# Kernel optimization log

Measured on AMD Instinct MI355X. Metric: run time of the kernel, lower is better.

## Reference

```python
import jax, jax.numpy as jnp
import numpy as np

N, L, IN = 256, 128, 8
H1, H2, OUT = 768, 512, 1


def setup_inputs() -> dict:
    key = jax.random.key(0)
    ks = jax.random.split(key, 13)
    s = 0.02
    p = lambda k, shape: jax.random.normal(k, shape, dtype=jnp.float32) * s
    return {
        "x": jax.random.normal(ks[0], (N, L, IN), dtype=jnp.float32),
        "W_ih1": p(ks[1], (4 * H1, IN + 1)),
        "b_ih1": p(ks[2], (4 * H1,)),
        "W_hh1": p(ks[3], (4 * H1, H1)),
        "b_hh1": p(ks[4], (4 * H1,)),
        "W_ih2": p(ks[5], (4 * H1, H1)),
        "b_ih2": p(ks[6], (4 * H1,)),
        "W_hh2": p(ks[7], (4 * H1, H1)),
        "b_hh2": p(ks[8], (4 * H1,)),
        "W1": p(ks[9], (H2, H1)),
        "b1": p(ks[10], (H2,)),
        "W2": p(ks[11], (OUT, H2)),
        "b2": p(ks[12], (OUT,)),
    }


def _lstm_cell(inp, h, c, W_ih, b_ih, W_hh, b_hh):
    # PyTorch LSTMCell: gates ordered (input, forget, cell, output)
    g = inp @ W_ih.T + b_ih + h @ W_hh.T + b_hh
    i, f, gg, o = jnp.split(g, 4, axis=-1)
    c = jax.nn.sigmoid(f) * c + jax.nn.sigmoid(i) * jnp.tanh(gg)
    h = jax.nn.sigmoid(o) * jnp.tanh(c)
    return h, c


def reference(x, W_ih1, b_ih1, W_hh1, b_hh1, W_ih2, b_ih2, W_hh2, b_hh2, W1, b1, W2, b2):
    Nb = x.shape[0]
    H = W_hh1.shape[1]
    z = jnp.zeros((Nb, H), x.dtype)
    col0 = jnp.zeros((Nb, 1), x.dtype)  # initial_output = initial_implied_storage = 0

    def step(carry, x_t):  # x_t: (N, IN)
        h1, c1, h2, c2, prev_out, prev_store = carry
        cur_store = prev_store + x_t[:, :1] - prev_out  # (N, 1)
        inp = jnp.concatenate([x_t, cur_store], axis=-1)  # (N, IN+1)
        h1, c1 = _lstm_cell(inp, h1, c1, W_ih1, b_ih1, W_hh1, b_hh1)
        h2, c2 = _lstm_cell(h1, h2, c2, W_ih2, b_ih2, W_hh2, b_hh2)
        # dropout_prob = 0 -> dropout layers are identity
        out = jax.nn.relu(h2 @ W1.T + b1) @ W2.T + b2  # (N, 1)
        return (h1, c1, h2, c2, out, cur_store), (out, cur_store)

    _, (outs, stores) = jax.lax.scan(step, (z, z, z, z, col0, col0), jnp.swapaxes(x, 0, 1))
    # (L, N, 1) -> (N, L, 1)
    return jnp.swapaxes(outs, 0, 1), jnp.swapaxes(stores, 0, 1)
```

## Files before the change

### kernel.cpp

```cpp
#include <hip/hip_runtime.h>

typedef unsigned short u16;
typedef unsigned int u32;
typedef __attribute__((ext_vector_type(8))) unsigned short ushort8;
typedef __attribute__((ext_vector_type(4))) float f32x4;
typedef __attribute__((ext_vector_type(2))) float f32x2;
typedef __attribute__((ext_vector_type(4))) unsigned int u32x4;
typedef __attribute__((ext_vector_type(8))) __bf16 bf16x8;

#define N_B 256
#define LSEQ 128
#define AROW 2304
#define NBLK 256

#define MFMA_B16(a, b, c) __builtin_amdgcn_mfma_f32_16x16x32_bf16( \
    __builtin_bit_cast(bf16x8, a), __builtin_bit_cast(bf16x8, b), c, 0, 0, 0)

#define GLLDS(gp, lp) __builtin_amdgcn_global_load_lds( \
    (const __attribute__((address_space(1))) void*)(gp), \
    (__attribute__((address_space(3))) void*)(lp), 16, 0, 0)
#define GLLDS_C(gp, lp) __builtin_amdgcn_global_load_lds( \
    (const __attribute__((address_space(1))) void*)(gp), \
    (__attribute__((address_space(3))) void*)(lp), 16, 0, 17)

#define ATOMIC_LD(p) __hip_atomic_load((p), __ATOMIC_RELAXED, __HIP_MEMORY_SCOPE_AGENT)
#define ATOMIC_ST(p, v) __hip_atomic_store((p), (v), __ATOMIC_RELAXED, __HIP_MEMORY_SCOPE_AGENT)

__device__ __forceinline__ void st16_sc(void* p, u32x4 v) {
  asm volatile("global_store_dwordx4 %0, %1, off sc0 sc1" :: "v"(p), "v"(v) : "memory");
}
#define LOADB(dst, gp) asm volatile("global_load_dwordx4 %0, %1, off" : "=v"(dst) : "v"(gp))
#define VMW(N) asm volatile("s_waitcnt vmcnt(" #N ")" ::: "memory")

#define OFF_BP2   0ull
#define SZ_BP2    (48ull*192*512*2)
#define OFF_BP1   (OFF_BP2 + SZ_BP2)
#define SZ_BP1    (24ull*192*512*2)
#define OFF_W1P   (OFF_BP1 + SZ_BP1)
#define SZ_W1P    (24ull*32*512*2)
#define OFF_WIH1T (OFF_W1P + SZ_W1P)
#define SZ_WIH1T  (9ull*3072*4)
#define OFF_BS1   (OFF_WIH1T + SZ_WIH1T)
#define OFF_BS2   (OFF_BS1 + 3072*4)
#define OFF_W8Q   (OFF_BS2 + 3072*4)
#define OFF_G1P   (OFF_W8Q + 3072*4)
#define SZ_G1P    (256ull*3072*4)
#define OFF_PBUF  (OFF_G1P + SZ_G1P)
#define SZ_PBUF   (256ull*8*4)
#define OFF_ZERO  (OFF_PBUF + SZ_PBUF)
#define OFF_ACAT  OFF_ZERO
#define SZ_ACAT   (256ull*2304*2)
#define OFF_C1    (OFF_ACAT + SZ_ACAT)
#define OFF_C2    (OFF_C1 + 256ull*768*4)
#define OFF_SB    (OFF_C2 + 256ull*768*4)
#define OFF_BAR   (OFF_SB + 1024)
#define SZ_BAR    (128 + 256*32*4)
#define OFF_END   (OFF_BAR + SZ_BAR)
#define ZERO_BYTES (OFF_END - OFF_ZERO)

__device__ __forceinline__ float sigf(float v) { return 1.f / (1.f + __expf(-v)); }
__device__ __forceinline__ float tanhfast(float v) { return 1.f - 2.f / (__expf(2.f * v) + 1.f); }
__device__ __forceinline__ u16 f2bf(float f) {
  union { float f; unsigned u; } v; v.f = f;
  unsigned r = v.u + 0x7fffu + ((v.u >> 16) & 1u);
  return (u16)(r >> 16);
}

struct Params {
  const float* x;
  const u16* Bp2; const u16* Bp1; const u16* W1p;
  const float* Wih1t; const float* bs1; const float* bs2; const float* w8q;
  const float* b1; const float* W2; const float* b2;
  u16* Acat; float* g1q; float* c1; float* c2; float* sb; float* pbuf;
  unsigned* bar;
  float* outs; float* stores;
};

__device__ __forceinline__ void waitflags(const unsigned* f, int n, unsigned target, int tid) {
  if (tid < 64) {
    for (;;) {
      unsigned v = (tid < n) ? ATOMIC_LD(f + tid) : target;
      if (__all((int)(v >= target))) break;
      __builtin_amdgcn_s_sleep(1);
    }
  }
  __syncthreads();
}
__device__ __forceinline__ void setflag(unsigned* f, unsigned v) {
  asm volatile("s_waitcnt vmcnt(0)" ::: "memory");
  __syncthreads();
  if (threadIdx.x == 0) ATOMIC_ST(f, v);
}

__global__ void pack_kernel(const float* __restrict__ Wih1, const float* __restrict__ bih1,
                            const float* __restrict__ Whh1, const float* __restrict__ bhh1,
                            const float* __restrict__ Wih2, const float* __restrict__ bih2,
                            const float* __restrict__ Whh2, const float* __restrict__ bhh2,
                            const float* __restrict__ W1,
                            u16* __restrict__ Bp2, u16* __restrict__ Bp1, u16* __restrict__ W1p,
                            float* __restrict__ Wih1t, float* __restrict__ bs1,
                            float* __restrict__ bs2, float* __restrict__ w8q) {
  const long NB2 = 48l * 192 * 512, NB1 = 24l * 192 * 512, NW1 = 24l * 32 * 512, NT = 9l * 3072;
  const long total = NB2 + NB1 + NW1 + NT + 3072 * 3;
  for (long idx = (long)blockIdx.x * 256 + threadIdx.x; idx < total; idx += (long)gridDim.x * 256) {
    if (idx < NB2) {
      long kt = idx / (192 * 512); long r = idx % (192 * 512);
      int jt = (int)(r / 512); int s = (int)(r % 512);
      int ll = s >> 3, e = s & 7;
      int k = (int)kt * 32 + ((ll >> 4) * 8) + e;
      int j = jt * 16 + (ll & 15);
      float v = (k < 768) ? Wih2[j * 768 + k] : Whh2[j * 768 + k - 768];
      Bp2[idx] = f2bf(v);
    } else if (idx < NB2 + NB1) {
      long i = idx - NB2;
      long kt = i / (192 * 512); long r = i % (192 * 512);
      int jt = (int)(r / 512); int s = (int)(r % 512);
      int ll = s >> 3, e = s & 7;
      int k = (int)kt * 32 + ((ll >> 4) * 8) + e;
      int j = jt * 16 + (ll & 15);
      Bp1[i] = f2bf(Whh1[j * 768 + k]);
    } else if (idx < NB2 + NB1 + NW1) {
      long i = idx - NB2 - NB1;
      long kt = i / (32 * 512); long r = i % (32 * 512);
      int jt = (int)(r / 512); int s = (int)(r % 512);
      int ll = s >> 3, e = s & 7;
      int k = (int)kt * 32 + ((ll >> 4) * 8) + e;
      int j = jt * 16 + (ll & 15);
      W1p[i] = f2bf(W1[j * 768 + k]);
    } else if (idx < NB2 + NB1 + NW1 + NT) {
      long i = idx - NB2 - NB1 - NW1;
      int k = (int)(i / 3072), j = (int)(i % 3072);
      Wih1t[i] = Wih1[j * 9 + k];
    } else {
      long i = idx - NB2 - NB1 - NW1 - NT;
      if (i < 3072) bs1[i] = bih1[i] + bhh1[i];
      else if (i < 6144) { long j = i - 3072; bs2[j] = bih2[j] + bhh2[j]; }
      else {
        long cq = i - 6144; int cc = (int)(cq >> 2), q = (int)(cq & 3);
        w8q[cq] = Wih1[(q * 768 + cc) * 9 + 8];
      }
    }
  }
}

__global__ __launch_bounds__(256) void lstm_fused(Params P) {
  __shared__ ushort8 sbuf[48 * 64];
  __shared__ float xsb[64][8];
  __shared__ float csh[8];
  float (*fbuf)[64][16] = (float(*)[64][16])sbuf;
  const int tid = threadIdx.x, l = tid & 63, w = tid >> 6;
  const int bid = blockIdx.x;
  const int c = bid >> 6, local = bid & 63;
  const int rowbase = c * 64;
  unsigned* cfl = P.bar + 32 + c * 128;

  if (local < 48) {
    const int mg = local;
    setflag(cfl + local, 1u);
    for (int t = 0; t < 128; ++t) {
      const int rdbase = 768 + (t & 1) * 768;
      const int wrbase = 768 + ((t + 1) & 1) * 768;
      waitflags(cfl, 48, (unsigned)(t + 1), tid);

      f32x4 acc[4] = {};
      ushort8 bring[4][2];
      auto issueA2 = [&](int gi) {
        const int slot = gi % 6;
#pragma unroll
        for (int kt2 = 0; kt2 < 2; ++kt2) {
          int kt = ((gi < 12) ? gi + 12 : gi - 12) * 2 + kt2;
          int col = (kt >= 24) ? (rdbase + (kt - 24) * 32 + ((l >> 4) * 8))
                               : (kt * 32 + ((l >> 4) * 8));
          const u16* gp = P.Acat + (rowbase + w * 16 + (l & 15)) * AROW + col;
          GLLDS_C(gp, &sbuf[slot * 512 + (kt2 * 4 + w) * 64]);
        }
      };
      auto baddr2 = [&](int gi, int kt2) -> const u16* {
        int kt = ((gi < 12) ? gi + 12 : gi - 12) * 2 + kt2;
        return P.Bp2 + (((long)(kt * 192 + w * 48 + mg)) << 9) + l * 8;
      };
      auto g2_step = [&](int g, const ushort8 (&bu)[2]) {
        __builtin_amdgcn_s_barrier();
        __builtin_amdgcn_sched_barrier(0);
        const int sb8 = (g % 6) * 512;
#pragma unroll
        for (int kt2 = 0; kt2 < 2; ++kt2)
#pragma unroll
          for (int rt = 0; rt < 4; ++rt) {
            ushort8 a = sbuf[sb8 + (kt2 * 4 + rt) * 64 + l];
            acc[rt] = MFMA_B16(a, bu[kt2], acc[rt]);
          }
        __builtin_amdgcn_sched_barrier(0);
      };
#pragma unroll
      for (int p = 0; p < 3; ++p) {
        issueA2(p);
        LOADB(bring[p][0], baddr2(p, 0));
        LOADB(bring[p][1], baddr2(p, 1));
      }
      for (int ko = 0; ko < 5; ++ko) {
#pragma unroll
        for (int u = 0; u < 4; ++u) {
          const int g = ko * 4 + u;
          if (g == 9) waitflags(cfl + 96, 16, (unsigned)(t + 1), tid);
          issueA2(g + 3);
          LOADB(bring[(u + 3) & 3][0], baddr2(g + 3, 0));
          LOADB(bring[(u + 3) & 3][1], baddr2(g + 3, 1));
          VMW(12);
          g2_step(g, bring[u]);
        }
      }
      issueA2(23);
      LOADB(bring[3][0], baddr2(23, 0));
      LOADB(bring[3][1], baddr2(23, 1));
      VMW(12); g2_step(20, bring[0]);
      VMW(8);  g2_step(21, bring[1]);
      VMW(4);  g2_step(22, bring[2]);
      VMW(0);  g2_step(23, bring[3]);
      __syncthreads();

#pragma unroll
      for (int rt = 0; rt < 4; ++rt)
#pragma unroll
        for (int reg = 0; reg < 4; ++reg) {
          int rl = rt * 16 + (l >> 4) * 4 + reg;
          fbuf[w][rl][l & 15] = acc[rt][reg] + P.bs2[w * 768 + mg * 16 + (l & 15)];
        }
      __syncthreads();
      for (int p = tid; p < 128; p += 256) {
        int r = p >> 1, half = p & 1;
        int n = rowbase + r, mG = mg * 16 + half * 8;
        f32x4 cold0 = *(const f32x4*)(P.c2 + n * 768 + mG);
        f32x4 cold1 = *(const f32x4*)(P.c2 + n * 768 + mG + 4);
        u32 hp[4];
        f32x4 cnew0, cnew1;
#pragma unroll
        for (int k = 0; k < 8; ++k) {
          int pp = half * 8 + k;
          float gi = fbuf[0][r][pp], gf = fbuf[1][r][pp], gg = fbuf[2][r][pp], go = fbuf[3][r][pp];
          float co = (k < 4) ? cold0[k] : cold1[k - 4];
          float cn = sigf(gf) * co + sigf(gi) * tanhfast(gg);
          float h = sigf(go) * tanhfast(cn);
          if (k < 4) cnew0[k] = cn; else cnew1[k - 4] = cn;
          if (k & 1) hp[k >> 1] |= ((u32)f2bf(h)) << 16; else hp[k >> 1] = f2bf(h);
        }
        *(f32x4*)(P.c2 + n * 768 + mG) = cnew0;
        *(f32x4*)(P.c2 + n * 768 + mG + 4) = cnew1;
        st16_sc(P.Acat + n * AROW + wrbase + mG, *(u32x4*)hp);
      }
      setflag(cfl + local, (unsigned)(t + 2));

      if (local < 32) {
        waitflags(cfl, 48, (unsigned)(t + 2), tid);
        ushort8* fst = sbuf + 1024;
        const int n0f = rowbase + (local >> 3) * 16, cg2 = local & 7, ctg = cg2 * 4 + w;
        const int h2rd = 768 + ((t + 1) & 1) * 768;
#pragma unroll
        for (int i = 0; i < 6; ++i) {
          int cc = w * 6 + i;
          const u16* gp = P.Acat + (n0f + (l & 15)) * AROW + h2rd + cc * 32 + ((l >> 4) * 8);
          GLLDS_C(gp, &fst[cc * 64]);
        }
        asm volatile("s_waitcnt vmcnt(0)" ::: "memory");
        __syncthreads();
        const u16* bbase = P.W1p + ((long)ctg << 9) + l * 8;
        f32x4 facc = {};
#pragma unroll 6
        for (int kt = 0; kt < 24; ++kt) {
          ushort8 a = fst[kt * 64 + l];
          ushort8 bf8 = *reinterpret_cast<const ushort8*>(bbase + kt * 16384);
          facc = MFMA_B16(a, bf8, facc);
        }
        int col = ctg * 16 + (l & 15);
        float w2v = P.W2[col], b1v = P.b1[col];
        float pr[4];
#pragma unroll
        for (int reg = 0; reg < 4; ++reg) pr[reg] = fmaxf(facc[reg] + b1v, 0.f) * w2v;
#pragma unroll
        for (int mm = 1; mm < 16; mm <<= 1)
#pragma unroll
          for (int reg = 0; reg < 4; ++reg) pr[reg] += __shfl_xor(pr[reg], mm);
        if ((l & 15) == 0)
#pragma unroll
          for (int reg = 0; reg < 4; ++reg) fbuf[w][(l >> 4) * 4 + reg][0] = pr[reg];
        __syncthreads();
        if (tid < 16)
          ATOMIC_ST(P.pbuf + (n0f + tid) * 8 + cg2,
                    fbuf[0][tid][0] + fbuf[1][tid][0] + fbuf[2][tid][0] + fbuf[3][tid][0]);
        setflag(cfl + 64 + local, (unsigned)(t + 2));
      }
    }
  } else {
    const int jb = local - 48;
    const int n0 = rowbase + jb * 4;
    for (int t = -1; t < 128; ++t) {
      float ov = 0.f;
      if (t < 127) {
        if (t >= 0) waitflags(cfl + 96, 16, (unsigned)(t + 1), tid);
        for (int p = tid; p < 512; p += 256)
          xsb[p >> 3][p & 7] = P.x[((rowbase + (p >> 3)) * LSEQ + t + 1) * 8 + (p & 7)];
        __syncthreads();
        f32x4 acc[3][4] = {};
        if (t >= 0) {
          ushort8 br1[4][3];
          auto issueA1 = [&](int ki) {
            const u16* gp = P.Acat + (rowbase + w * 16 + (l & 15)) * AROW + ki * 32 + ((l >> 4) * 8);
            GLLDS_C(gp, &sbuf[(ki & 7) * 256 + w * 64]);
          };
          auto baddr1 = [&](int ki, int jj) -> const u16* {
            return P.Bp1 + (((long)(ki * 192 + w * 48 + jb * 3 + jj)) << 9) + l * 8;
          };
          auto g1_step = [&](int kt, const ushort8 (&bu)[3]) {
            __builtin_amdgcn_s_barrier();
            __builtin_amdgcn_sched_barrier(0);
            const int sb8 = (kt & 7) * 256;
            ushort8 a_[4];
#pragma unroll
            for (int rt = 0; rt < 4; ++rt) a_[rt] = sbuf[sb8 + rt * 64 + l];
#pragma unroll
            for (int jj = 0; jj < 3; ++jj)
#pragma unroll
              for (int rt = 0; rt < 4; ++rt)
                acc[jj][rt] = MFMA_B16(a_[rt], bu[jj], acc[jj][rt]);
            __builtin_amdgcn_sched_barrier(0);
          };
#pragma unroll
          for (int p = 0; p < 3; ++p) {
            issueA1(p);
            LOADB(br1[p][0], baddr1(p, 0));
            LOADB(br1[p][1], baddr1(p, 1));
            LOADB(br1[p][2], baddr1(p, 2));
          }
          for (int ko = 0; ko < 5; ++ko) {
#pragma unroll
            for (int u = 0; u < 4; ++u) {
              const int kt = ko * 4 + u;
              issueA1(kt + 3);
              LOADB(br1[(u + 3) & 3][0], baddr1(kt + 3, 0));
              LOADB(br1[(u + 3) & 3][1], baddr1(kt + 3, 1));
              LOADB(br1[(u + 3) & 3][2], baddr1(kt + 3, 2));
              VMW(12);
              g1_step(kt, br1[u]);
            }
          }
          issueA1(23);
          LOADB(br1[3][0], baddr1(23, 0));
          LOADB(br1[3][1], baddr1(23, 1));
          LOADB(br1[3][2], baddr1(23, 2));
          VMW(12); g1_step(20, br1[0]);
          VMW(8);  g1_step(21, br1[1]);
          VMW(4);  g1_step(22, br1[2]);
          VMW(0);  g1_step(23, br1[3]);
          __syncthreads();
        }
        float wc[3][8], bsv[3];
#pragma unroll
        for (int jj = 0; jj < 3; ++jj) {
          int j = w * 768 + (jb * 3 + jj) * 16 + (l & 15);
          bsv[jj] = P.bs1[j];
#pragma unroll
          for (int k = 0; k < 8; ++k) wc[jj][k] = P.Wih1t[k * 3072 + j];
        }
        float* eps = (float*)sbuf;
#pragma unroll
        for (int rt = 0; rt < 4; ++rt)
#pragma unroll
          for (int reg = 0; reg < 4; ++reg) {
            int rl = rt * 16 + (l >> 4) * 4 + reg;
            float xv[8];
#pragma unroll
            for (int k = 0; k < 8; ++k) xv[k] = xsb[rl][k];
#pragma unroll
            for (int jj = 0; jj < 3; ++jj) {
              float v = acc[jj][rt][reg] + bsv[jj];
#pragma unroll
              for (int k = 0; k < 8; ++k) v += xv[k] * wc[jj][k];
              eps[rl * 192 + (jj * 16 + (l & 15)) * 4 + w] = v;
            }
          }
        __syncthreads();
#pragma unroll
        for (int k2 = 0; k2 < 12; ++k2) {
          int idx = tid + k2 * 256;
          int row = idx / 48, cl = idx - row * 48;
          u32x4 v = *(const u32x4*)(eps + row * 192 + cl * 4);
          st16_sc(P.g1q + (rowbase + row) * 3072 + (jb * 48 + cl) * 4, v);
        }
        setflag(cfl + 48 + jb, (unsigned)(t + 2));

        waitflags(cfl + 48, 16, (unsigned)(t + 2), tid);
#pragma unroll
        for (int i = 0; i < 12; ++i) {
          int f = w * 12 + i;
          const float* gp = P.g1q + n0 * 3072 + f * 256 + l * 4;
          GLLDS_C(gp, (char*)sbuf + f * 1024);
        }
      }

      if (t >= 0) {
        waitflags(cfl + 64, 32, (unsigned)(t + 2), tid);
        if (tid < 4) {
          int n = n0 + tid;
          float pb[8];
#pragma unroll
          for (int i = 0; i < 8; ++i) pb[i] = ATOMIC_LD(P.pbuf + n * 8 + i);
          ov = ((pb[0] + pb[1]) + (pb[2] + pb[3])) + ((pb[4] + pb[5]) + (pb[6] + pb[7])) + P.b2[0];
          P.outs[n * LSEQ + t] = ov;
        }
      }
      if (t < 127) {
        if (tid < 4) {
          int n = n0 + tid;
          float cs = P.sb[n] + P.x[(n * LSEQ + t + 1) * 8] - ov;
          P.sb[n] = cs;
          P.stores[n * LSEQ + t + 1] = cs;
          csh[tid] = cs;
        }
        asm volatile("s_waitcnt vmcnt(0)" ::: "memory");
        __syncthreads();
        const int r = tid >> 6, l2 = tid & 63;
        const int n = n0 + r;
        const float* ldsrow = (const float*)sbuf + r * 3072;
        float cs = csh[r];
        for (int idx = l2; idx < 96; idx += 64) {
          int m = idx * 8;
          u32 hp[4];
          f32x4 c1v0 = *(const f32x4*)(P.c1 + n * 768 + m);
          f32x4 c1v1 = *(const f32x4*)(P.c1 + n * 768 + m + 4);
          f32x4 nc0, nc1;
#pragma unroll
          for (int k = 0; k < 8; ++k) {
            int mm = m + k;
            f32x4 q = *(const f32x4*)(ldsrow + mm * 4);
            f32x4 wq = *(const f32x4*)(P.w8q + mm * 4);
            float g0 = q[0] + cs * wq[0], g1v = q[1] + cs * wq[1];
            float g2v = q[2] + cs * wq[2], g3v = q[3] + cs * wq[3];
            float co = (k < 4) ? c1v0[k] : c1v1[k - 4];
            float cn = sigf(g1v) * co + sigf(g0) * tanhfast(g2v);
            float h = sigf(g3v) * tanhfast(cn);
            if (k < 4) nc0[k] = cn; else nc1[k - 4] = cn;
            if (k & 1) hp[k >> 1] |= ((u32)f2bf(h)) << 16; else hp[k >> 1] = f2bf(h);
          }
          *(f32x4*)(P.c1 + n * 768 + m) = nc0;
          *(f32x4*)(P.c1 + n * 768 + m + 4) = nc1;
          st16_sc(P.Acat + n * AROW + m, *(u32x4*)hp);
        }
        setflag(cfl + 96 + jb, (unsigned)(t + 2));
      }
    }
  }
}

extern "C" void kernel_launch(void* const* d_in, const int* in_sizes, int n_in,
                              void* d_out, int out_size, void* d_ws, size_t ws_size,
                              hipStream_t stream) {
  const float* x    = (const float*)d_in[0];
  const float* Wih1 = (const float*)d_in[1];
  const float* bih1 = (const float*)d_in[2];
  const float* Whh1 = (const float*)d_in[3];
  const float* bhh1 = (const float*)d_in[4];
  const float* Wih2 = (const float*)d_in[5];
  const float* bih2 = (const float*)d_in[6];
  const float* Whh2 = (const float*)d_in[7];
  const float* bhh2 = (const float*)d_in[8];
  const float* W1   = (const float*)d_in[9];
  const float* b1   = (const float*)d_in[10];
  const float* W2   = (const float*)d_in[11];
  const float* b2   = (const float*)d_in[12];

  char* ws = (char*)d_ws;
  u16* Bp2 = (u16*)(ws + OFF_BP2);
  u16* Bp1 = (u16*)(ws + OFF_BP1);
  u16* W1p = (u16*)(ws + OFF_W1P);
  float* Wih1t = (float*)(ws + OFF_WIH1T);
  float* bs1 = (float*)(ws + OFF_BS1);
  float* bs2 = (float*)(ws + OFF_BS2);
  float* w8q = (float*)(ws + OFF_W8Q);
  float* g1q = (float*)(ws + OFF_G1P);
  float* pbuf = (float*)(ws + OFF_PBUF);
  u16* Acat = (u16*)(ws + OFF_ACAT);
  float* c1 = (float*)(ws + OFF_C1);
  float* c2 = (float*)(ws + OFF_C2);
  float* sb = (float*)(ws + OFF_SB);
  unsigned* bar = (unsigned*)(ws + OFF_BAR);
  float* outs = (float*)d_out;
  float* stores = outs + N_B * LSEQ;

  pack_kernel<<<2048, 256, 0, stream>>>(Wih1, bih1, Whh1, bhh1, Wih2, bih2, Whh2, bhh2, W1,
                                        Bp2, Bp1, W1p, Wih1t, bs1, bs2, w8q);
  (void)hipMemsetAsync(ws + OFF_ZERO, 0, ZERO_BYTES, stream);

  Params Pr = {x, Bp2, Bp1, W1p, Wih1t, bs1, bs2, w8q, b1, W2, b2,
               Acat, g1q, c1, c2, sb, pbuf, bar, outs, stores};
  lstm_fused<<<NBLK, 256, 0, stream>>>(Pr);
}
```

Measured before the change: 3.159 ms.

## Deepen GEMM prefetch ring, swizzle gate LDS reads, narrow output flag wait

```diff
diff --git a/kernel.cpp b/kernel.cpp
--- a/kernel.cpp
+++ b/kernel.cpp
@@ -179,21 +179,24 @@
         int kt = ((gi < 12) ? gi + 12 : gi - 12) * 2 + kt2;
         return P.Bp2 + (((long)(kt * 192 + w * 48 + mg)) << 9) + l * 8;
       };
-      auto g2_step = [&](int g, const ushort8 (&bu)[2]) {
+      auto g2_step = [&](int g, ushort8 b0, ushort8 b1) {
         __builtin_amdgcn_s_barrier();
         __builtin_amdgcn_sched_barrier(0);
         const int sb8 = (g % 6) * 512;
 #pragma unroll
-        for (int kt2 = 0; kt2 < 2; ++kt2)
-#pragma unroll
-          for (int rt = 0; rt < 4; ++rt) {
-            ushort8 a = sbuf[sb8 + (kt2 * 4 + rt) * 64 + l];
-            acc[rt] = MFMA_B16(a, bu[kt2], acc[rt]);
-          }
+        for (int rt = 0; rt < 4; ++rt) {
+          ushort8 a = sbuf[sb8 + rt * 64 + l];
+          acc[rt] = MFMA_B16(a, b0, acc[rt]);
+        }
+#pragma unroll
+        for (int rt = 0; rt < 4; ++rt) {
+          ushort8 a = sbuf[sb8 + (4 + rt) * 64 + l];
+          acc[rt] = MFMA_B16(a, b1, acc[rt]);
+        }
         __builtin_amdgcn_sched_barrier(0);
       };
 #pragma unroll
-      for (int p = 0; p < 3; ++p) {
+      for (int p = 0; p < 4; ++p) {
         issueA2(p);
         LOADB(bring[p][0], baddr2(p, 0));
         LOADB(bring[p][1], baddr2(p, 1));
@@ -202,21 +205,19 @@
 #pragma unroll
         for (int u = 0; u < 4; ++u) {
           const int g = ko * 4 + u;
-          if (g == 9) waitflags(cfl + 96, 16, (unsigned)(t + 1), tid);
-          issueA2(g + 3);
-          LOADB(bring[(u + 3) & 3][0], baddr2(g + 3, 0));
-          LOADB(bring[(u + 3) & 3][1], baddr2(g + 3, 1));
-          VMW(12);
-          g2_step(g, bring[u]);
-        }
-      }
-      issueA2(23);
-      LOADB(bring[3][0], baddr2(23, 0));
-      LOADB(bring[3][1], baddr2(23, 1));
-      VMW(12); g2_step(20, bring[0]);
-      VMW(8);  g2_step(21, bring[1]);
-      VMW(4);  g2_step(22, bring[2]);
-      VMW(0);  g2_step(23, bring[3]);
+          if (g == 8) waitflags(cfl + 96, 16, (unsigned)(t + 1), tid);
+          ushort8 b0 = bring[u][0], b1 = bring[u][1];
+          issueA2(g + 4);
+          LOADB(bring[u][0], baddr2(g + 4, 0));
+          LOADB(bring[u][1], baddr2(g + 4, 1));
+          VMW(16);
+          g2_step(g, b0, b1);
+        }
+      }
+      VMW(12); g2_step(20, bring[0][0], bring[0][1]);
+      VMW(8);  g2_step(21, bring[1][0], bring[1][1]);
+      VMW(4);  g2_step(22, bring[2][0], bring[2][1]);
+      VMW(0);  g2_step(23, bring[3][0], bring[3][1]);
       __syncthreads();
 
 #pragma unroll
@@ -310,7 +311,7 @@
           auto baddr1 = [&](int ki, int jj) -> const u16* {
             return P.Bp1 + (((long)(ki * 192 + w * 48 + jb * 3 + jj)) << 9) + l * 8;
           };
-          auto g1_step = [&](int kt, const ushort8 (&bu)[3]) {
+          auto g1_step = [&](int kt, ushort8 b0, ushort8 b1, ushort8 b2) {
             __builtin_amdgcn_s_barrier();
             __builtin_amdgcn_sched_barrier(0);
             const int sb8 = (kt & 7) * 256;
@@ -318,14 +319,15 @@
 #pragma unroll
             for (int rt = 0; rt < 4; ++rt) a_[rt] = sbuf[sb8 + rt * 64 + l];
 #pragma unroll
-            for (int jj = 0; jj < 3; ++jj)
-#pragma unroll
-              for (int rt = 0; rt < 4; ++rt)
-                acc[jj][rt] = MFMA_B16(a_[rt], bu[jj], acc[jj][rt]);
+            for (int rt = 0; rt < 4; ++rt) acc[0][rt] = MFMA_B16(a_[rt], b0, acc[0][rt]);
+#pragma unroll
+            for (int rt = 0; rt < 4; ++rt) acc[1][rt] = MFMA_B16(a_[rt], b1, acc[1][rt]);
+#pragma unroll
+            for (int rt = 0; rt < 4; ++rt) acc[2][rt] = MFMA_B16(a_[rt], b2, acc[2][rt]);
             __builtin_amdgcn_sched_barrier(0);
           };
 #pragma unroll
-          for (int p = 0; p < 3; ++p) {
+          for (int p = 0; p < 4; ++p) {
             issueA1(p);
             LOADB(br1[p][0], baddr1(p, 0));
             LOADB(br1[p][1], baddr1(p, 1));
@@ -335,22 +337,19 @@
 #pragma unroll
             for (int u = 0; u < 4; ++u) {
               const int kt = ko * 4 + u;
-              issueA1(kt + 3);
-              LOADB(br1[(u + 3) & 3][0], baddr1(kt + 3, 0));
-              LOADB(br1[(u + 3) & 3][1], baddr1(kt + 3, 1));
-              LOADB(br1[(u + 3) & 3][2], baddr1(kt + 3, 2));
-              VMW(12);
-              g1_step(kt, br1[u]);
+              ushort8 b0 = br1[u][0], b1 = br1[u][1], b2 = br1[u][2];
+              issueA1(kt + 4);
+              LOADB(br1[u][0], baddr1(kt + 4, 0));
+              LOADB(br1[u][1], baddr1(kt + 4, 1));
+              LOADB(br1[u][2], baddr1(kt + 4, 2));
+              VMW(20);
+              g1_step(kt, b0, b1, b2);
             }
           }
-          issueA1(23);
-          LOADB(br1[3][0], baddr1(23, 0));
-          LOADB(br1[3][1], baddr1(23, 1));
-          LOADB(br1[3][2], baddr1(23, 2));
-          VMW(12); g1_step(20, br1[0]);
-          VMW(8);  g1_step(21, br1[1]);
-          VMW(4);  g1_step(22, br1[2]);
-          VMW(0);  g1_step(23, br1[3]);
+          VMW(15); g1_step(20, br1[0][0], br1[0][1], br1[0][2]);
+          VMW(10); g1_step(21, br1[1][0], br1[1][1], br1[1][2]);
+          VMW(5);  g1_step(22, br1[2][0], br1[2][1], br1[2][2]);
+          VMW(0);  g1_step(23, br1[3][0], br1[3][1], br1[3][2]);
           __syncthreads();
         }
         float wc[3][8], bsv[3];
@@ -392,13 +391,13 @@
 #pragma unroll
         for (int i = 0; i < 12; ++i) {
           int f = w * 12 + i;
-          const float* gp = P.g1q + n0 * 3072 + f * 256 + l * 4;
+          const float* gp = P.g1q + n0 * 3072 + ((f * 256 + l * 4) ^ (((l >> 3) & 7) << 2));
           GLLDS_C(gp, (char*)sbuf + f * 1024);
         }
       }
 
       if (t >= 0) {
-        waitflags(cfl + 64, 32, (unsigned)(t + 2), tid);
+        waitflags(cfl + 64 + (jb >> 2) * 8, 8, (unsigned)(t + 2), tid);
         if (tid < 4) {
           int n = n0 + tid;
           float pb[8];
@@ -431,7 +430,7 @@
 #pragma unroll
           for (int k = 0; k < 8; ++k) {
             int mm = m + k;
-            f32x4 q = *(const f32x4*)(ldsrow + mm * 4);
+            f32x4 q = *(const f32x4*)(ldsrow + ((mm * 4) ^ (((mm >> 3) & 7) << 2)));
             f32x4 wq = *(const f32x4*)(P.w8q + mm * 4);
             float g0 = q[0] + cs * wq[0], g1v = q[1] + cs * wq[1];
             float g2v = q[2] + cs * wq[2], g3v = q[3] + cs * wq[3];
```

Result: slower. 3.230 ms (+2.2%).
